# Kernel optimization log

Measured on AMD Instinct MI355X. Metric: run time of the kernel, lower is better.

The kernel has to match this reference:

```python
import jax, jax.numpy as jnp
import numpy as np

N = 50000        # nodes
E = 1600000      # edges (before self loops)
IN = 128         # in_channels
HID = 32         # hidden_channels
HEADS = 4
OUT = 16         # out_channels
B = 512          # graphs in batch
NEG_SLOPE = 0.2  # PyG GATConv default


def _uniform(key, shape, fan_in):
    s = 1.0 / np.sqrt(fan_in)
    return jax.random.uniform(key, shape, jnp.float32, -s, s)


def setup_inputs() -> dict:
    key = jax.random.key(0)
    ks = jax.random.split(key, 12)
    x = jax.random.normal(ks[0], (N, IN), jnp.float32)
    edge_index = jax.random.randint(ks[1], (2, E), 0, N, dtype=jnp.int64)
    batch = jnp.sort(jax.random.randint(ks[2], (N,), 0, B, dtype=jnp.int64))
    return {
        "x": x,
        "edge_index": edge_index,
        "batch": batch,
        "W1": _uniform(ks[3], (IN, HEADS * HID), IN),
        "att_src": _uniform(ks[4], (HEADS, HID), HID),
        "att_dst": _uniform(ks[5], (HEADS, HID), HID),
        "b1": jnp.zeros((HEADS * HID,), jnp.float32),
        "lin1_w": _uniform(ks[6], (HEADS * HID, HID), HEADS * HID),
        "lin1_b": _uniform(ks[7], (HID,), HEADS * HID),
        "lin2_w": _uniform(ks[8], (HID, OUT), HID),
        "lin2_b": _uniform(ks[9], (OUT,), HID),
    }


def _gat_conv(x, src, dst, W1, att_src, att_dst, b1):
    # h: [N, H, C]
    h = (x @ W1).reshape(N, HEADS, HID)
    a_s = (h * att_src).sum(-1)   # [N, H]
    a_d = (h * att_dst).sum(-1)   # [N, H]
    # per-edge attention logits [E', H]
    alpha = jax.nn.leaky_relu(a_s[src] + a_d[dst], negative_slope=NEG_SLOPE)
    # segment softmax over incoming edges of each destination node
    amax = jax.lax.stop_gradient(jax.ops.segment_max(alpha, dst, num_segments=N))
    ex = jnp.exp(alpha - amax[dst])
    den = jax.ops.segment_sum(ex, dst, num_segments=N)
    a = ex / (den[dst] + 1e-16)
    # weighted scatter-aggregate of source features: [N, H, C]
    out = jax.ops.segment_sum(h[src] * a[:, :, None], dst, num_segments=N)
    return out.reshape(N, HEADS * HID) + b1


def reference(x, edge_index, batch, W1, att_src, att_dst, b1, lin1_w, lin1_b, lin2_w, lin2_b):
    # add self loops (PyG GATConv default add_self_loops=True)
    loop = jnp.arange(N, dtype=edge_index.dtype)
    src = jnp.concatenate([edge_index[0], loop])
    dst = jnp.concatenate([edge_index[1], loop])
    # dropout layers are identity in eval mode
    xh = jax.nn.elu(_gat_conv(x, src, dst, W1, att_src, att_dst, b1))
    g = jax.ops.segment_sum(xh, batch, num_segments=B)  # global_add_pool -> [B, H*C]
    g = g @ lin1_w + lin1_b
    return g @ lin2_w + lin2_b
```

## Files before the change

kernel.cpp:

```cpp
#include <hip/hip_runtime.h>
#include <hip/hip_bf16.h>
#include <hip/hip_fp16.h>

#define N_NODES 50000
#define E_EDGES 1600000
#define IN_CH 128
#define HID 32
#define HEADS 4
#define HC (HEADS * HID)
#define OUT_CH 16
#define B_GRAPHS 512
#define NEG_SLOPE 0.2f
#define CAP 96
#define NB 512
#define BNODES 98
#define PCAP 3552
#define ACHUNK 4096
#define APART 391
#define ROWS_PB 64
#define GEMM_BLOCKS 782
#define TOT_BLOCKS 1173

typedef short bfrag __attribute__((ext_vector_type(8)));
typedef float facc  __attribute__((ext_vector_type(4)));

__device__ __forceinline__ unsigned short f2bf(float f) {
    unsigned int u = __float_as_uint(f);
    unsigned int r = (u + 0x7FFFu + ((u >> 16) & 1u)) >> 16;
    return (unsigned short)r;
}

__device__ __forceinline__ float lrelu_exp(float v) {
    v = v > 0.f ? v : NEG_SLOPE * v;
    return __expf(v);
}

__global__ __launch_bounds__(256) void k_prep(const float* __restrict__ W1,
                                              unsigned short* __restrict__ whiF,
                                              unsigned short* __restrict__ wloF,
                                              int* __restrict__ gcur) {
    int tid = blockIdx.x * 256 + threadIdx.x;
    if (tid < NB) gcur[tid] = 0;
    int e = tid & 7, l = (tid >> 3) & 63, q = tid >> 9;
    int nt = q >> 2, kc = q & 3;
    int n = nt * 16 + (l & 15);
    int k = kc * 32 + (l >> 4) * 8 + e;
    float v = W1[k * 128 + n];
    unsigned int u = __float_as_uint(v);
    float lo_f = v - __uint_as_float(u & 0xFFFF0000u);
    whiF[tid] = (unsigned short)(u >> 16);
    wloF[tid] = f2bf(lo_f);
}

__global__ __launch_bounds__(256) void k_fused(const float* __restrict__ x,
                                               const unsigned short* __restrict__ whiF,
                                               const unsigned short* __restrict__ wloF,
                                               const float* __restrict__ att_src,
                                               const float* __restrict__ att_dst,
                                               const int* __restrict__ ei,
                                               unsigned short* __restrict__ hb,
                                               float* __restrict__ a_s,
                                               float* __restrict__ a_d,
                                               int* __restrict__ gcur,
                                               unsigned int* __restrict__ ebuf,
                                               float* __restrict__ g) {
    __shared__ float smem[8256];
    const int t = threadIdx.x;
    const int bI = blockIdx.x;

    if (bI % 3 == 0) {
        const int ablk = bI / 3;
        int* scnt = (int*)smem;
        int* sbase = scnt + 4 * NB;
        const int wv = t >> 6;
        const int e0 = ablk * ACHUNK;
        int e1 = e0 + ACHUNK; if (e1 > E_EDGES) e1 = E_EDGES;
        for (int i = t; i < 4 * NB; i += 256) scnt[i] = 0;
        __syncthreads();
        const int* __restrict__ dstp = ei + E_EDGES;
        for (int e = e0 + t; e < e1; e += 256) {
            int d = dstp[e];
            atomicAdd(&scnt[wv * NB + d / BNODES], 1);
        }
        __syncthreads();
        for (int i = t; i < NB; i += 256) {
            int c0 = scnt[0 * NB + i], c1 = scnt[1 * NB + i];
            int c2 = scnt[2 * NB + i], c3 = scnt[3 * NB + i];
            int base = atomicAdd(&gcur[i], c0 + c1 + c2 + c3);
            sbase[0 * NB + i] = base;
            sbase[1 * NB + i] = base + c0;
            sbase[2 * NB + i] = base + c0 + c1;
            sbase[3 * NB + i] = base + c0 + c1 + c2;
            scnt[0 * NB + i] = 0; scnt[1 * NB + i] = 0;
            scnt[2 * NB + i] = 0; scnt[3 * NB + i] = 0;
        }
        __syncthreads();
        for (int e = e0 + t; e < e1; e += 256) {
            int d = dstp[e];
            int s = ei[e];
            int b = d / BNODES;
            int dl = d - b * BNODES;
            int pos = sbase[wv * NB + b] + atomicAdd(&scnt[wv * NB + b], 1);
            if (pos < PCAP)
                ebuf[(size_t)b * PCAP + pos] = ((unsigned int)dl << 16) | (unsigned int)s;
        }
        return;
    }

    unsigned short* sxh = (unsigned short*)smem;
    unsigned short* sxl = sxh + 64 * 128;
    const int bid = bI - bI / 3 - 1;
    const int n0 = bid * ROWS_PB;

    int gt = bid * 256 + t;
    if (gt < B_GRAPHS * HC) g[gt] = 0.f;

    for (int it = 0; it < 8; it++) {
        int i = t + it * 256;
        int r = i >> 5, c4 = i & 31;
        int n = n0 + r;
        float4 v = (n < N_NODES) ? ((const float4*)x)[(size_t)n * 32 + c4]
                                 : make_float4(0.f, 0.f, 0.f, 0.f);
        unsigned int ux = __float_as_uint(v.x), uy = __float_as_uint(v.y);
        unsigned int uz = __float_as_uint(v.z), uw = __float_as_uint(v.w);
        unsigned int uh0 = (ux >> 16) | (uy & 0xFFFF0000u);
        unsigned int uh1 = (uz >> 16) | (uw & 0xFFFF0000u);
        float lx = v.x - __uint_as_float(ux & 0xFFFF0000u);
        float ly = v.y - __uint_as_float(uy & 0xFFFF0000u);
        float lz = v.z - __uint_as_float(uz & 0xFFFF0000u);
        float lw = v.w - __uint_as_float(uw & 0xFFFF0000u);
        unsigned int ul0 = (unsigned int)f2bf(lx) | ((unsigned int)f2bf(ly) << 16);
        unsigned int ul1 = (unsigned int)f2bf(lz) | ((unsigned int)f2bf(lw) << 16);
        int byo = r * 256 + (((c4 >> 1) ^ (r & 7)) << 4) + (c4 & 1) * 8;
        *(uint2*)((char*)sxh + byo) = make_uint2(uh0, uh1);
        *(uint2*)((char*)sxl + byo) = make_uint2(ul0, ul1);
    }
    __syncthreads();

    const int wv = t >> 6, l = t & 63;
    const int lm = l & 15, lk = l >> 4;
    const int band = wv * 16;

    bfrag ahi[4], alo[4];
    {
        int row = band + lm;
#pragma unroll
        for (int kc = 0; kc < 4; kc++) {
            int sl = (kc * 4 + lk) ^ (row & 7);
            ahi[kc] = *(const bfrag*)((const char*)sxh + row * 256 + sl * 16);
            alo[kc] = *(const bfrag*)((const char*)sxl + row * 256 + sl * 16);
        }
    }

    facc acc[8];
#pragma unroll
    for (int nt = 0; nt < 8; nt++) acc[nt] = (facc){0.f, 0.f, 0.f, 0.f};

    {
        const int lb = l * 8;
#pragma unroll
        for (int nt = 0; nt < 8; nt++) {
#pragma unroll
            for (int kc = 0; kc < 4; kc++) {
                bfrag bhv = *(const bfrag*)(whiF + (nt * 4 + kc) * 512 + lb);
                bfrag blv = *(const bfrag*)(wloF + (nt * 4 + kc) * 512 + lb);
                acc[nt] = __builtin_amdgcn_mfma_f32_16x16x32_bf16(ahi[kc], bhv, acc[nt], 0, 0, 0);
                acc[nt] = __builtin_amdgcn_mfma_f32_16x16x32_bf16(alo[kc], bhv, acc[nt], 0, 0, 0);
                acc[nt] = __builtin_amdgcn_mfma_f32_16x16x32_bf16(ahi[kc], blv, acc[nt], 0, 0, 0);
            }
        }
    }

    __syncthreads();
    float* sH = smem;
#pragma unroll
    for (int nt = 0; nt < 8; nt++) {
#pragma unroll
        for (int r = 0; r < 4; r++)
            sH[(band + lk * 4 + r) * 129 + nt * 16 + lm] = acc[nt][r];
    }
    __syncthreads();

    for (int i = t; i < 64 * 32; i += 256) {
        int row = i >> 5, c4 = i & 31;
        const float* p = &sH[row * 129 + c4 * 4];
        int n = n0 + row;
        if (n < N_NODES) {
            ushort4 o;
            o.x = f2bf(p[0]); o.y = f2bf(p[1]);
            o.z = f2bf(p[2]); o.w = f2bf(p[3]);
            *(ushort4*)&hb[(size_t)n * HC + c4 * 4] = o;
        }
    }

    if (t < 128) {
        int r = t & 63;
        int n = n0 + r;
        const float* __restrict__ av = (t < 64) ? att_src : att_dst;
        float s0 = 0.f, s1 = 0.f, s2 = 0.f, s3 = 0.f;
#pragma unroll 4
        for (int j = 0; j < 32; j++) {
            const float* row = &sH[r * 129 + j];
            s0 += row[0]  * av[j];
            s1 += row[32] * av[32 + j];
            s2 += row[64] * av[64 + j];
            s3 += row[96] * av[96 + j];
        }
        if (n < N_NODES) {
            float* dst = (t < 64) ? a_s : a_d;
            *(float4*)(dst + (size_t)n * 4) = make_float4(s0, s1, s2, s3);
        }
    }
}

#define NPW 7
__global__ __launch_bounds__(1024) void k_aggB(const unsigned int* __restrict__ ebuf,
                                               const int* __restrict__ gcur,
                                               const float* __restrict__ a_s,
                                               const float* __restrict__ a_d,
                                               const unsigned short* __restrict__ hb,
                                               const float* __restrict__ b1,
                                               const int* __restrict__ batch,
                                               float* __restrict__ g) {
    __shared__ unsigned short sbuf[BNODES * CAP];
    __shared__ int scnt[BNODES];
    __shared__ float sWt[16][4][97];
    const int t = threadIdx.x;
    const int b = blockIdx.x;
    const int dbase = b * BNODES;

    for (int i = t; i < BNODES; i += 1024) {
        int d = dbase + i;
        scnt[i] = (d < N_NODES) ? 1 : 0;
        sbuf[i * CAP] = (unsigned short)d;
    }
    __syncthreads();
    int m = gcur[b]; if (m > PCAP) m = PCAP;
    for (int i = t; i < m; i += 1024) {
        unsigned int p = ebuf[(size_t)b * PCAP + i];
        int dl = p >> 16;
        int s = p & 0xFFFFu;
        int c = atomicAdd(&scnt[dl], 1);
        if (c < CAP) sbuf[dl * CAP + c] = (unsigned short)s;
    }
    __syncthreads();

    const int wv = t >> 6;
    const int l = t & 63;
    const int head = l >> 4;
    const int c0 = 2 * l;
    int nl0 = wv * NPW;
    if (nl0 >= BNODES) return;
    int nl1 = nl0 + NPW; if (nl1 > BNODES) nl1 = BNODES;
    int gn0 = dbase + nl0;
    if (gn0 >= N_NODES) return;
    int gn1 = dbase + nl1; if (gn1 > N_NODES) gn1 = N_NODES;
    const float2 bias = *(const float2*)(b1 + c0);
    float pool0 = 0.f, pool1 = 0.f;
    int cur = batch[gn0];
    for (int n = gn0; n < gn1; n++) {
        int bb = batch[n];
        if (bb != cur) {
            atomicAdd(&g[(size_t)cur * HC + c0], pool0);
            atomicAdd(&g[(size_t)cur * HC + c0 + 1], pool1);
            pool0 = pool1 = 0.f;
            cur = bb;
        }
        int nl = n - dbase;
        int c = scnt[nl]; if (c > CAP) c = CAP;
        float4 ad = *(const float4*)(a_d + (size_t)n * 4);
        const unsigned short* __restrict__ srow = &sbuf[nl * CAP];
        for (int i = l; i < c; i += 64) {
            int s = srow[i];
            float4 as = *(const float4*)(a_s + (size_t)s * 4);
            sWt[wv][0][i] = lrelu_exp(as.x + ad.x);
            sWt[wv][1][i] = lrelu_exp(as.y + ad.y);
            sWt[wv][2][i] = lrelu_exp(as.z + ad.z);
            sWt[wv][3][i] = lrelu_exp(as.w + ad.w);
        }
        __asm__ volatile("" ::: "memory");
        const float* __restrict__ wrow = &sWt[wv][head][0];
        float acc0 = 0.f, acc1 = 0.f, dsum = 0.f;
        int i = 0;
        for (; i + 8 <= c; i += 8) {
            unsigned int u[8];
            float w[8];
#pragma unroll
            for (int q = 0; q < 8; q++) {
                int sq = srow[i + q];
                w[q] = wrow[i + q];
                u[q] = *(const unsigned int*)(hb + (size_t)sq * HC + c0);
            }
#pragma unroll
            for (int q = 0; q < 8; q++) {
                dsum += w[q];
                acc0 += w[q] * __uint_as_float(u[q] << 16);
                acc1 += w[q] * __uint_as_float(u[q] & 0xFFFF0000u);
            }
        }
        for (; i < c; i++) {
            int s0 = srow[i];
            float w0 = wrow[i];
            unsigned int u0 = *(const unsigned int*)(hb + (size_t)s0 * HC + c0);
            dsum += w0;
            acc0 += w0 * __uint_as_float(u0 << 16);
            acc1 += w0 * __uint_as_float(u0 & 0xFFFF0000u);
        }
        __asm__ volatile("" ::: "memory");
        float inv = 1.f / (dsum + 1e-16f);
        float v0 = acc0 * inv + bias.x; v0 = v0 > 0.f ? v0 : (__expf(v0) - 1.f);
        float v1 = acc1 * inv + bias.y; v1 = v1 > 0.f ? v1 : (__expf(v1) - 1.f);
        pool0 += v0;
        pool1 += v1;
    }
    atomicAdd(&g[(size_t)cur * HC + c0], pool0);
    atomicAdd(&g[(size_t)cur * HC + c0 + 1], pool1);
}

__global__ __launch_bounds__(64) void k_mlp(const float* __restrict__ g,
                                            const float* __restrict__ w1,
                                            const float* __restrict__ bb1,
                                            const float* __restrict__ w2,
                                            const float* __restrict__ bb2,
                                            float* __restrict__ out) {
    __shared__ float sg[HC];
    __shared__ float st[HID];
    int b = blockIdx.x;
    int t = threadIdx.x;
    sg[t]      = g[(size_t)b * HC + t];
    sg[t + 64] = g[(size_t)b * HC + 64 + t];
    __syncthreads();
    if (t < HID) {
        float acc = bb1[t];
#pragma unroll 8
        for (int k = 0; k < HC; k++) acc += sg[k] * w1[(size_t)k * HID + t];
        st[t] = acc;
    }
    __syncthreads();
    if (t < OUT_CH) {
        float acc = bb2[t];
#pragma unroll
        for (int k = 0; k < HID; k++) acc += st[k] * w2[(size_t)k * OUT_CH + t];
        out[(size_t)b * OUT_CH + t] = acc;
    }
}

extern "C" void kernel_launch(void* const* d_in, const int* in_sizes, int n_in,
                              void* d_out, int out_size, void* d_ws, size_t ws_size,
                              hipStream_t stream) {
    const float* x       = (const float*)d_in[0];
    const int*   ei      = (const int*)d_in[1];
    const int*   batch   = (const int*)d_in[2];
    const float* W1      = (const float*)d_in[3];
    const float* att_src = (const float*)d_in[4];
    const float* att_dst = (const float*)d_in[5];
    const float* b1      = (const float*)d_in[6];
    const float* lin1_w  = (const float*)d_in[7];
    const float* lin1_b  = (const float*)d_in[8];
    const float* lin2_w  = (const float*)d_in[9];
    const float* lin2_b  = (const float*)d_in[10];
    float* out = (float*)d_out;

    float* ws = (float*)d_ws;
    unsigned short* hb   = (unsigned short*)ws;
    float*  a_s      = ws + 3200000;
    float*  a_d      = ws + 3400000;
    unsigned int* ebuf = (unsigned int*)(ws + 3600000);
    unsigned short* whiF = (unsigned short*)(ws + 5418624);
    unsigned short* wloF = (unsigned short*)(ws + 5426816);
    int*    gcur     = (int*)(ws + 5435008);
    float*  g        = ws + 5436000;

    k_prep<<<64, 256, 0, stream>>>(W1, whiF, wloF, gcur);
    k_fused<<<TOT_BLOCKS, 256, 0, stream>>>(
        x, whiF, wloF, att_src, att_dst, ei, hb, a_s, a_d, gcur, ebuf, g);
    k_aggB<<<NB, 1024, 0, stream>>>(ebuf, gcur, a_s, a_d, hb, b1, batch, g);
    k_mlp<<<B_GRAPHS, 64, 0, stream>>>(g, lin1_w, lin1_b, lin2_w, lin2_b, out);
}
```

Before: 192.7 us.

## Fuse MLP head into aggregation kernel via last-block ticket and prefetch GEMM weights

The final MLP kernel is removed. Its work now runs inside the aggregation kernel, in whichever block is the last to finish, found with an atomic ticket counter that k_prep zeroes. This drops one kernel launch and the gap before it, at the cost of running the MLP serially in a single block after a threadfence. The MFMA loop in the fused GEMM is also restructured into a flat loop that prefetches the weight fragments three steps ahead, to hide global load latency.

New measurement: 448.4 us. +132.6%, slower.

```diff
diff --git a/kernel.cpp b/kernel.cpp
--- a/kernel.cpp
+++ b/kernel.cpp
@@ -40,7 +40,7 @@
                                               unsigned short* __restrict__ wloF,
                                               int* __restrict__ gcur) {
     int tid = blockIdx.x * 256 + threadIdx.x;
-    if (tid < NB) gcur[tid] = 0;
+    if (tid <= NB) gcur[tid] = 0;
     int e = tid & 7, l = (tid >> 3) & 63, q = tid >> 9;
     int nt = q >> 2, kc = q & 3;
     int n = nt * 16 + (l & 15);
@@ -158,16 +158,22 @@
 
     {
         const int lb = l * 8;
-#pragma unroll
-        for (int nt = 0; nt < 8; nt++) {
-#pragma unroll
-            for (int kc = 0; kc < 4; kc++) {
-                bfrag bhv = *(const bfrag*)(whiF + (nt * 4 + kc) * 512 + lb);
-                bfrag blv = *(const bfrag*)(wloF + (nt * 4 + kc) * 512 + lb);
-                acc[nt] = __builtin_amdgcn_mfma_f32_16x16x32_bf16(ahi[kc], bhv, acc[nt], 0, 0, 0);
-                acc[nt] = __builtin_amdgcn_mfma_f32_16x16x32_bf16(alo[kc], bhv, acc[nt], 0, 0, 0);
-                acc[nt] = __builtin_amdgcn_mfma_f32_16x16x32_bf16(ahi[kc], blv, acc[nt], 0, 0, 0);
+        bfrag bh[4], bl[4];
+#pragma unroll
+        for (int q = 0; q < 3; q++) {
+            bh[q] = *(const bfrag*)(whiF + q * 512 + lb);
+            bl[q] = *(const bfrag*)(wloF + q * 512 + lb);
+        }
+#pragma unroll
+        for (int q = 0; q < 32; q++) {
+            if (q + 3 < 32) {
+                bh[(q + 3) & 3] = *(const bfrag*)(whiF + (q + 3) * 512 + lb);
+                bl[(q + 3) & 3] = *(const bfrag*)(wloF + (q + 3) * 512 + lb);
             }
+            const int nt = q >> 2, kc = q & 3;
+            acc[nt] = __builtin_amdgcn_mfma_f32_16x16x32_bf16(ahi[kc], bh[kc & 3], acc[nt], 0, 0, 0);
+            acc[nt] = __builtin_amdgcn_mfma_f32_16x16x32_bf16(alo[kc], bh[kc & 3], acc[nt], 0, 0, 0);
+            acc[nt] = __builtin_amdgcn_mfma_f32_16x16x32_bf16(ahi[kc], bl[kc & 3], acc[nt], 0, 0, 0);
         }
     }
 
@@ -221,10 +227,17 @@
                                                const unsigned short* __restrict__ hb,
                                                const float* __restrict__ b1,
                                                const int* __restrict__ batch,
-                                               float* __restrict__ g) {
+                                               float* __restrict__ g,
+                                               int* __restrict__ ticket,
+                                               const float* __restrict__ lin1_w,
+                                               const float* __restrict__ lin1_b,
+                                               const float* __restrict__ lin2_w,
+                                               const float* __restrict__ lin2_b,
+                                               float* __restrict__ out) {
     __shared__ unsigned short sbuf[BNODES * CAP];
     __shared__ int scnt[BNODES];
     __shared__ float sWt[16][4][97];
+    __shared__ int slast;
     const int t = threadIdx.x;
     const int b = blockIdx.x;
     const int dbase = b * BNODES;
@@ -250,98 +263,109 @@
     const int head = l >> 4;
     const int c0 = 2 * l;
     int nl0 = wv * NPW;
-    if (nl0 >= BNODES) return;
-    int nl1 = nl0 + NPW; if (nl1 > BNODES) nl1 = BNODES;
     int gn0 = dbase + nl0;
-    if (gn0 >= N_NODES) return;
-    int gn1 = dbase + nl1; if (gn1 > N_NODES) gn1 = N_NODES;
-    const float2 bias = *(const float2*)(b1 + c0);
-    float pool0 = 0.f, pool1 = 0.f;
-    int cur = batch[gn0];
-    for (int n = gn0; n < gn1; n++) {
-        int bb = batch[n];
-        if (bb != cur) {
-            atomicAdd(&g[(size_t)cur * HC + c0], pool0);
-            atomicAdd(&g[(size_t)cur * HC + c0 + 1], pool1);
-            pool0 = pool1 = 0.f;
-            cur = bb;
-        }
-        int nl = n - dbase;
-        int c = scnt[nl]; if (c > CAP) c = CAP;
-        float4 ad = *(const float4*)(a_d + (size_t)n * 4);
-        const unsigned short* __restrict__ srow = &sbuf[nl * CAP];
-        for (int i = l; i < c; i += 64) {
-            int s = srow[i];
-            float4 as = *(const float4*)(a_s + (size_t)s * 4);
-            sWt[wv][0][i] = lrelu_exp(as.x + ad.x);
-            sWt[wv][1][i] = lrelu_exp(as.y + ad.y);
-            sWt[wv][2][i] = lrelu_exp(as.z + ad.z);
-            sWt[wv][3][i] = lrelu_exp(as.w + ad.w);
-        }
-        __asm__ volatile("" ::: "memory");
-        const float* __restrict__ wrow = &sWt[wv][head][0];
-        float acc0 = 0.f, acc1 = 0.f, dsum = 0.f;
-        int i = 0;
-        for (; i + 8 <= c; i += 8) {
-            unsigned int u[8];
-            float w[8];
-#pragma unroll
-            for (int q = 0; q < 8; q++) {
-                int sq = srow[i + q];
-                w[q] = wrow[i + q];
-                u[q] = *(const unsigned int*)(hb + (size_t)sq * HC + c0);
+    const bool active = (nl0 < BNODES) && (gn0 < N_NODES);
+    if (active) {
+        int nl1 = nl0 + NPW; if (nl1 > BNODES) nl1 = BNODES;
+        int gn1 = dbase + nl1; if (gn1 > N_NODES) gn1 = N_NODES;
+        const float2 bias = *(const float2*)(b1 + c0);
+        float pool0 = 0.f, pool1 = 0.f;
+        int cur = batch[gn0];
+        for (int n = gn0; n < gn1; n++) {
+            int bb = batch[n];
+            if (bb != cur) {
+                atomicAdd(&g[(size_t)cur * HC + c0], pool0);
+                atomicAdd(&g[(size_t)cur * HC + c0 + 1], pool1);
+                pool0 = pool1 = 0.f;
+                cur = bb;
             }
-#pragma unroll
-            for (int q = 0; q < 8; q++) {
-                dsum += w[q];
-                acc0 += w[q] * __uint_as_float(u[q] << 16);
-                acc1 += w[q] * __uint_as_float(u[q] & 0xFFFF0000u);
+            int nl = n - dbase;
+            int c = scnt[nl]; if (c > CAP) c = CAP;
+            float4 ad = *(const float4*)(a_d + (size_t)n * 4);
+            const unsigned short* __restrict__ srow = &sbuf[nl * CAP];
+            for (int i = l; i < c; i += 64) {
+                int s = srow[i];
+                float4 as = *(const float4*)(a_s + (size_t)s * 4);
+                sWt[wv][0][i] = lrelu_exp(as.x + ad.x);
+                sWt[wv][1][i] = lrelu_exp(as.y + ad.y);
+                sWt[wv][2][i] = lrelu_exp(as.z + ad.z);
+                sWt[wv][3][i] = lrelu_exp(as.w + ad.w);
             }
-        }
-        for (; i < c; i++) {
-            int s0 = srow[i];
-            float w0 = wrow[i];
-            unsigned int u0 = *(const unsigned int*)(hb + (size_t)s0 * HC + c0);
-            dsum += w0;
-            acc0 += w0 * __uint_as_float(u0 << 16);
-            acc1 += w0 * __uint_as_float(u0 & 0xFFFF0000u);
-        }
-        __asm__ volatile("" ::: "memory");
-        float inv = 1.f / (dsum + 1e-16f);
-        float v0 = acc0 * inv + bias.x; v0 = v0 > 0.f ? v0 : (__expf(v0) - 1.f);
-        float v1 = acc1 * inv + bias.y; v1 = v1 > 0.f ? v1 : (__expf(v1) - 1.f);
-        pool0 += v0;
-        pool1 += v1;
-    }
-    atomicAdd(&g[(size_t)cur * HC + c0], pool0);
-    atomicAdd(&g[(size_t)cur * HC + c0 + 1], pool1);
-}
-
-__global__ __launch_bounds__(64) void k_mlp(const float* __restrict__ g,
-                                            const float* __restrict__ w1,
-                                            const float* __restrict__ bb1,
-                                            const float* __restrict__ w2,
-                                            const float* __restrict__ bb2,
-                                            float* __restrict__ out) {
-    __shared__ float sg[HC];
-    __shared__ float st[HID];
-    int b = blockIdx.x;
-    int t = threadIdx.x;
-    sg[t]      = g[(size_t)b * HC + t];
-    sg[t + 64] = g[(size_t)b * HC + 64 + t];
-    __syncthreads();
-    if (t < HID) {
-        float acc = bb1[t];
+            __asm__ volatile("" ::: "memory");
+            const float* __restrict__ wrow = &sWt[wv][head][0];
+            float acc0 = 0.f, acc1 = 0.f, dsum = 0.f;
+            int i = 0;
+            for (; i + 8 <= c; i += 8) {
+                unsigned int u[8];
+                float w[8];
+#pragma unroll
+                for (int q = 0; q < 8; q++) {
+                    int sq = srow[i + q];
+                    w[q] = wrow[i + q];
+                    u[q] = *(const unsigned int*)(hb + (size_t)sq * HC + c0);
+                }
+#pragma unroll
+                for (int q = 0; q < 8; q++) {
+                    dsum += w[q];
+                    acc0 += w[q] * __uint_as_float(u[q] << 16);
+                    acc1 += w[q] * __uint_as_float(u[q] & 0xFFFF0000u);
+                }
+            }
+            for (; i < c; i++) {
+                int s0 = srow[i];
+                float w0 = wrow[i];
+                unsigned int u0 = *(const unsigned int*)(hb + (size_t)s0 * HC + c0);
+                dsum += w0;
+                acc0 += w0 * __uint_as_float(u0 << 16);
+                acc1 += w0 * __uint_as_float(u0 & 0xFFFF0000u);
+            }
+            __asm__ volatile("" ::: "memory");
+            float inv = 1.f / (dsum + 1e-16f);
+            float v0 = acc0 * inv + bias.x; v0 = v0 > 0.f ? v0 : (__expf(v0) - 1.f);
+            float v1 = acc1 * inv + bias.y; v1 = v1 > 0.f ? v1 : (__expf(v1) - 1.f);
+            pool0 += v0;
+            pool1 += v1;
+        }
+        atomicAdd(&g[(size_t)cur * HC + c0], pool0);
+        atomicAdd(&g[(size_t)cur * HC + c0 + 1], pool1);
+    }
+
+    __threadfence();
+    __syncthreads();
+    if (t == 0) slast = (atomicAdd(ticket, 1) == NB - 1) ? 1 : 0;
+    __syncthreads();
+    if (!slast) return;
+
+    float* sw1  = (float*)sbuf;
+    float* sg2  = &sWt[0][0][0];
+    float* shid = sg2 + 32 * HC;
+    for (int i = t; i < HC * HID; i += 1024) sw1[i] = lin1_w[i];
+    __syncthreads();
+    const int gl = t >> 5;
+    const int h  = t & 31;
+    for (int chunk = 0; chunk < B_GRAPHS / 32; chunk++) {
+        int gbase = chunk * 32;
+        for (int i = t; i < 32 * HC; i += 1024) {
+            int gi = gbase + (i >> 7);
+            sg2[i] = __hip_atomic_load(&g[(size_t)gi * HC + (i & 127)],
+                                       __ATOMIC_RELAXED, __HIP_MEMORY_SCOPE_AGENT);
+        }
+        __syncthreads();
+        float acc = lin1_b[h];
 #pragma unroll 8
-        for (int k = 0; k < HC; k++) acc += sg[k] * w1[(size_t)k * HID + t];
-        st[t] = acc;
-    }
-    __syncthreads();
-    if (t < OUT_CH) {
-        float acc = bb2[t];
-#pragma unroll
-        for (int k = 0; k < HID; k++) acc += st[k] * w2[(size_t)k * OUT_CH + t];
-        out[(size_t)b * OUT_CH + t] = acc;
+        for (int k = 0; k < HC; k++)
+            acc += sg2[gl * HC + k] * sw1[k * HID + h];
+        shid[gl * HID + h] = acc;
+        __syncthreads();
+        if (t < 32 * OUT_CH) {
+            int gi2 = t >> 4, o = t & 15;
+            float a2 = lin2_b[o];
+#pragma unroll
+            for (int k = 0; k < HID; k++)
+                a2 += shid[gi2 * HID + k] * lin2_w[k * OUT_CH + o];
+            out[(size_t)(gbase + gi2) * OUT_CH + o] = a2;
+        }
+        __syncthreads();
     }
 }
 
@@ -374,6 +398,6 @@
     k_prep<<<64, 256, 0, stream>>>(W1, whiF, wloF, gcur);
     k_fused<<<TOT_BLOCKS, 256, 0, stream>>>(
         x, whiF, wloF, att_src, att_dst, ei, hb, a_s, a_d, gcur, ebuf, g);
-    k_aggB<<<NB, 1024, 0, stream>>>(ebuf, gcur, a_s, a_d, hb, b1, batch, g);
-    k_mlp<<<B_GRAPHS, 64, 0, stream>>>(g, lin1_w, lin1_b, lin2_w, lin2_b, out);
-}
+    k_aggB<<<NB, 1024, 0, stream>>>(ebuf, gcur, a_s, a_d, hb, b1, batch, g,
+                                    gcur + NB, lin1_w, lin1_b, lin2_w, lin2_b, out);
+}
```

## Split fused bucketing/GEMM kernel into separate passes and fold weight prep

Applied to the files above, without the earlier changes.

Replaces the single interleaved kernel, where every third block bucketed edges and the rest ran the GEMM, with two kernels. The first buckets edges and also does the W1 hi/lo bf16 split in its first 64 blocks. The second runs only the MFMA GEMM, and its nested nt/kc loop is flattened into one 32-step loop. The gcur reset moves to a hipMemsetAsync. This removes branch divergence and the shared-memory footprint mismatch between block types, at the cost of losing overlap between bucketing and the GEMM and adding a memset.

New measurement: 198.7 us. +3.1%, slower.

```diff
diff --git a/kernel.cpp b/kernel.cpp
--- a/kernel.cpp
+++ b/kernel.cpp
@@ -19,7 +19,7 @@
 #define APART 391
 #define ROWS_PB 64
 #define GEMM_BLOCKS 782
-#define TOT_BLOCKS 1173
+
 
 typedef short bfrag __attribute__((ext_vector_type(8)));
 typedef float facc  __attribute__((ext_vector_type(4)));
@@ -35,81 +35,79 @@
     return __expf(v);
 }
 
-__global__ __launch_bounds__(256) void k_prep(const float* __restrict__ W1,
-                                              unsigned short* __restrict__ whiF,
-                                              unsigned short* __restrict__ wloF,
-                                              int* __restrict__ gcur) {
-    int tid = blockIdx.x * 256 + threadIdx.x;
-    if (tid < NB) gcur[tid] = 0;
-    int e = tid & 7, l = (tid >> 3) & 63, q = tid >> 9;
-    int nt = q >> 2, kc = q & 3;
-    int n = nt * 16 + (l & 15);
-    int k = kc * 32 + (l >> 4) * 8 + e;
-    float v = W1[k * 128 + n];
-    unsigned int u = __float_as_uint(v);
-    float lo_f = v - __uint_as_float(u & 0xFFFF0000u);
-    whiF[tid] = (unsigned short)(u >> 16);
-    wloF[tid] = f2bf(lo_f);
-}
-
-__global__ __launch_bounds__(256) void k_fused(const float* __restrict__ x,
-                                               const unsigned short* __restrict__ whiF,
-                                               const unsigned short* __restrict__ wloF,
-                                               const float* __restrict__ att_src,
-                                               const float* __restrict__ att_dst,
-                                               const int* __restrict__ ei,
-                                               unsigned short* __restrict__ hb,
-                                               float* __restrict__ a_s,
-                                               float* __restrict__ a_d,
+__global__ __launch_bounds__(256) void k_passA(const int* __restrict__ ei,
+                                               const float* __restrict__ W1,
+                                               unsigned short* __restrict__ whiF,
+                                               unsigned short* __restrict__ wloF,
                                                int* __restrict__ gcur,
-                                               unsigned int* __restrict__ ebuf,
-                                               float* __restrict__ g) {
+                                               unsigned int* __restrict__ ebuf) {
+    __shared__ int smemA[8 * NB];
+    const int t = threadIdx.x;
+    const int ablk = blockIdx.x;
+
+    if (ablk < 64) {
+        int tid = ablk * 256 + t;
+        int e = tid & 7, l = (tid >> 3) & 63, q = tid >> 9;
+        int nt = q >> 2, kc = q & 3;
+        int n = nt * 16 + (l & 15);
+        int k = kc * 32 + (l >> 4) * 8 + e;
+        float v = W1[k * 128 + n];
+        unsigned int u = __float_as_uint(v);
+        float lo_f = v - __uint_as_float(u & 0xFFFF0000u);
+        whiF[tid] = (unsigned short)(u >> 16);
+        wloF[tid] = f2bf(lo_f);
+    }
+
+    int* scnt = smemA;
+    int* sbase = scnt + 4 * NB;
+    const int wv = t >> 6;
+    const int e0 = ablk * ACHUNK;
+    int e1 = e0 + ACHUNK; if (e1 > E_EDGES) e1 = E_EDGES;
+    for (int i = t; i < 4 * NB; i += 256) scnt[i] = 0;
+    __syncthreads();
+    const int* __restrict__ dstp = ei + E_EDGES;
+    for (int e = e0 + t; e < e1; e += 256) {
+        int d = dstp[e];
+        atomicAdd(&scnt[wv * NB + d / BNODES], 1);
+    }
+    __syncthreads();
+    for (int i = t; i < NB; i += 256) {
+        int c0 = scnt[0 * NB + i], c1 = scnt[1 * NB + i];
+        int c2 = scnt[2 * NB + i], c3 = scnt[3 * NB + i];
+        int base = atomicAdd(&gcur[i], c0 + c1 + c2 + c3);
+        sbase[0 * NB + i] = base;
+        sbase[1 * NB + i] = base + c0;
+        sbase[2 * NB + i] = base + c0 + c1;
+        sbase[3 * NB + i] = base + c0 + c1 + c2;
+        scnt[0 * NB + i] = 0; scnt[1 * NB + i] = 0;
+        scnt[2 * NB + i] = 0; scnt[3 * NB + i] = 0;
+    }
+    __syncthreads();
+    for (int e = e0 + t; e < e1; e += 256) {
+        int d = dstp[e];
+        int s = ei[e];
+        int b = d / BNODES;
+        int dl = d - b * BNODES;
+        int pos = sbase[wv * NB + b] + atomicAdd(&scnt[wv * NB + b], 1);
+        if (pos < PCAP)
+            ebuf[(size_t)b * PCAP + pos] = ((unsigned int)dl << 16) | (unsigned int)s;
+    }
+}
+
+__global__ __launch_bounds__(256) void k_gemm(const float* __restrict__ x,
+                                              const unsigned short* __restrict__ whiF,
+                                              const unsigned short* __restrict__ wloF,
+                                              const float* __restrict__ att_src,
+                                              const float* __restrict__ att_dst,
+                                              unsigned short* __restrict__ hb,
+                                              float* __restrict__ a_s,
+                                              float* __restrict__ a_d,
+                                              float* __restrict__ g) {
     __shared__ float smem[8256];
     const int t = threadIdx.x;
-    const int bI = blockIdx.x;
-
-    if (bI % 3 == 0) {
-        const int ablk = bI / 3;
-        int* scnt = (int*)smem;
-        int* sbase = scnt + 4 * NB;
-        const int wv = t >> 6;
-        const int e0 = ablk * ACHUNK;
-        int e1 = e0 + ACHUNK; if (e1 > E_EDGES) e1 = E_EDGES;
-        for (int i = t; i < 4 * NB; i += 256) scnt[i] = 0;
-        __syncthreads();
-        const int* __restrict__ dstp = ei + E_EDGES;
-        for (int e = e0 + t; e < e1; e += 256) {
-            int d = dstp[e];
-            atomicAdd(&scnt[wv * NB + d / BNODES], 1);
-        }
-        __syncthreads();
-        for (int i = t; i < NB; i += 256) {
-            int c0 = scnt[0 * NB + i], c1 = scnt[1 * NB + i];
-            int c2 = scnt[2 * NB + i], c3 = scnt[3 * NB + i];
-            int base = atomicAdd(&gcur[i], c0 + c1 + c2 + c3);
-            sbase[0 * NB + i] = base;
-            sbase[1 * NB + i] = base + c0;
-            sbase[2 * NB + i] = base + c0 + c1;
-            sbase[3 * NB + i] = base + c0 + c1 + c2;
-            scnt[0 * NB + i] = 0; scnt[1 * NB + i] = 0;
-            scnt[2 * NB + i] = 0; scnt[3 * NB + i] = 0;
-        }
-        __syncthreads();
-        for (int e = e0 + t; e < e1; e += 256) {
-            int d = dstp[e];
-            int s = ei[e];
-            int b = d / BNODES;
-            int dl = d - b * BNODES;
-            int pos = sbase[wv * NB + b] + atomicAdd(&scnt[wv * NB + b], 1);
-            if (pos < PCAP)
-                ebuf[(size_t)b * PCAP + pos] = ((unsigned int)dl << 16) | (unsigned int)s;
-        }
-        return;
-    }
-
     unsigned short* sxh = (unsigned short*)smem;
     unsigned short* sxl = sxh + 64 * 128;
-    const int bid = bI - bI / 3 - 1;
+    const int bid = blockIdx.x;
     const int n0 = bid * ROWS_PB;
 
     int gt = bid * 256 + t;
@@ -159,15 +157,13 @@
     {
         const int lb = l * 8;
 #pragma unroll
-        for (int nt = 0; nt < 8; nt++) {
-#pragma unroll
-            for (int kc = 0; kc < 4; kc++) {
-                bfrag bhv = *(const bfrag*)(whiF + (nt * 4 + kc) * 512 + lb);
-                bfrag blv = *(const bfrag*)(wloF + (nt * 4 + kc) * 512 + lb);
-                acc[nt] = __builtin_amdgcn_mfma_f32_16x16x32_bf16(ahi[kc], bhv, acc[nt], 0, 0, 0);
-                acc[nt] = __builtin_amdgcn_mfma_f32_16x16x32_bf16(alo[kc], bhv, acc[nt], 0, 0, 0);
-                acc[nt] = __builtin_amdgcn_mfma_f32_16x16x32_bf16(ahi[kc], blv, acc[nt], 0, 0, 0);
-            }
+        for (int q = 0; q < 32; q++) {
+            bfrag bhv = *(const bfrag*)(whiF + q * 512 + lb);
+            bfrag blv = *(const bfrag*)(wloF + q * 512 + lb);
+            const int nt = q >> 2, kc = q & 3;
+            acc[nt] = __builtin_amdgcn_mfma_f32_16x16x32_bf16(ahi[kc], bhv, acc[nt], 0, 0, 0);
+            acc[nt] = __builtin_amdgcn_mfma_f32_16x16x32_bf16(alo[kc], bhv, acc[nt], 0, 0, 0);
+            acc[nt] = __builtin_amdgcn_mfma_f32_16x16x32_bf16(ahi[kc], blv, acc[nt], 0, 0, 0);
         }
     }
 
@@ -371,9 +367,10 @@
     int*    gcur     = (int*)(ws + 5435008);
     float*  g        = ws + 5436000;
 
-    k_prep<<<64, 256, 0, stream>>>(W1, whiF, wloF, gcur);
-    k_fused<<<TOT_BLOCKS, 256, 0, stream>>>(
-        x, whiF, wloF, att_src, att_dst, ei, hb, a_s, a_d, gcur, ebuf, g);
+    hipMemsetAsync(gcur, 0, NB * sizeof(int), stream);
+    k_passA<<<APART, 256, 0, stream>>>(ei, W1, whiF, wloF, gcur, ebuf);
+    k_gemm<<<GEMM_BLOCKS, 256, 0, stream>>>(
+        x, whiF, wloF, att_src, att_dst, hb, a_s, a_d, g);
     k_aggB<<<NB, 1024, 0, stream>>>(ebuf, gcur, a_s, a_d, hb, b1, batch, g);
     k_mlp<<<B_GRAPHS, 64, 0, stream>>>(g, lin1_w, lin1_b, lin2_w, lin2_b, out);
 }
```
